# Kernel tuning notes

Hardware: AMD Instinct MI355X
Metric: run time of the kernel (lower is better)

Reference implementation:

```python
import jax, jax.numpy as jnp
import numpy as np

HIDDEN = 300
N_HEADS = 4
DEPTH = 4
N_ATOMS = 30000
N_BONDS = 60000
MAX_NB = 6
N_MOLS = 600
ATOMS_PER_MOL = 50
ATOM_FDIM = 144
BOND_IN = ATOM_FDIM + 14  # 158
W_SCALE = 0.05


def setup_inputs() -> dict:
    key = jax.random.key(0)
    ks = jax.random.split(key, 12)
    rn = lambda k, shp: jax.random.normal(k, shp, dtype=jnp.float32)
    return {
        'fatoms': rn(ks[0], (N_ATOMS, ATOM_FDIM)),
        'fbonds': rn(ks[1], (N_BONDS, BOND_IN)),
        'agraph': jax.random.randint(ks[2], (N_ATOMS, MAX_NB), 0, N_BONDS, dtype=jnp.int32),
        'bgraph': jax.random.randint(ks[3], (N_BONDS, MAX_NB), 0, N_BONDS, dtype=jnp.int32),
        'W_i': rn(ks[4], (HIDDEN, BOND_IN)) * W_SCALE,
        'W_ma': rn(ks[5], (N_HEADS, HIDDEN, HIDDEN)) * W_SCALE,
        'W_h': rn(ks[6], (HIDDEN, N_HEADS * HIDDEN)) * W_SCALE,
        'W_o': rn(ks[7], (HIDDEN, ATOM_FDIM + HIDDEN)) * W_SCALE,
        'b_o': rn(ks[8], (HIDDEN,)) * W_SCALE,
        'W_a': rn(ks[9], (HIDDEN, HIDDEN)) * W_SCALE,
        'W_b': rn(ks[10], (HIDDEN, HIDDEN)) * W_SCALE,
        'b_b': rn(ks[11], (HIDDEN,)) * W_SCALE,
    }


def reference(fatoms, fbonds, agraph, bgraph, W_i, W_ma, W_h, W_o, b_o, W_a, W_b, b_b):
    E, K = bgraph.shape
    NH = W_ma.shape[0]
    H = W_i.shape[0]

    binput = fbonds @ W_i.T                      # [E, H]
    message = jax.nn.relu(binput)
    for _ in range(DEPTH - 1):
        nei = message[bgraph]                    # [E, K, H] gather over neighbor bonds
        # per-head attention scores: <W_ma[n] @ nei_ek, message_e>
        mt = jnp.einsum('eh,nhd->ned', message, W_ma)        # [NH, E, H]
        scores = jnp.einsum('ekd,ned->nek', nei, mt)         # [NH, E, K]
        w = jax.nn.softmax(scores, axis=2)
        comp = jnp.einsum('nek,ekh->enh', w, nei)            # [E, NH, H]
        nei_msg = comp.reshape(E, NH * H) @ W_h.T            # [E, H]
        message = jax.nn.relu(binput + nei_msg)              # dropout(p=0) = identity

    a_nei = message[agraph].sum(axis=1)          # [A, H] gather-sum incoming bonds
    ainput = jnp.concatenate([fatoms, a_nei], axis=1)
    atom_hiddens = jax.nn.relu(ainput @ W_o.T + b_o)         # [A, H]

    # uniform scope: N_MOLS molecules of ATOMS_PER_MOL atoms each
    cur = atom_hiddens.reshape(N_MOLS, ATOMS_PER_MOL, H)
    att_w = jax.nn.softmax(jnp.einsum('mah,mbh->mab', cur @ W_a.T, cur), axis=2)
    att_h = jax.nn.relu(jnp.einsum('mab,mbh->mah', att_w, cur) @ W_b.T + b_b)
    mol_vecs = (cur + att_h).sum(axis=1) / ATOMS_PER_MOL     # [N_MOLS, H]
    return mol_vecs
```

## Files before the change

### kernel.cpp

```cpp
#include <hip/hip_runtime.h>
#include <hip/hip_bf16.h>
#include <math.h>

#define HID       300
#define HP        320
#define NH        4
#define E_BONDS   60000
#define NATOMS    30000
#define KNB       6
#define NMOLS     600
#define APM       50
#define AFD       144
#define BONDIN    158

typedef unsigned short u16;
typedef unsigned int   u32;
typedef _Float16 f16;
typedef f16   f16x8 __attribute__((ext_vector_type(8)));
typedef float f32x4 __attribute__((ext_vector_type(4)));

__device__ inline float hlo(u32 u) { union { u32 i; f16 h[2]; } c; c.i = u; return (float)c.h[0]; }
__device__ inline float hhi(u32 u) { union { u32 i; f16 h[2]; } c; c.i = u; return (float)c.h[1]; }
__device__ inline u32 packh2(float a, float b) {
    union { u32 i; f16 h[2]; } c; c.h[0] = (f16)a; c.h[1] = (f16)b; return c.i;
}

__device__ inline void gl2lds16(const void* g, void* l) {
    __builtin_amdgcn_global_load_lds(
        (const __attribute__((address_space(1))) void*)g,
        (__attribute__((address_space(3))) void*)l, 16, 0, 0);
}

template <int BN, int EPI>
__global__ __launch_bounds__(256) void mfma_gemm_k(
    const f16* __restrict__ A, int lda,
    const f16* __restrict__ B, int ldb,
    int M, int Nb, int K, int ldc,
    float* __restrict__ Cf, f16* __restrict__ Ch,
    const float* __restrict__ bias,
    const f16* __restrict__ resid,
    f16* __restrict__ out2)
{
    constexpr int NF = BN / 32;
    __shared__ f16 sA[128 * 64];
    __shared__ f16 sB[BN * 64];
    const int tid  = threadIdx.x;
    const int lane = tid & 63;
    const int wv   = tid >> 6;
    const int wm   = wv >> 1, wn = wv & 1;
    const int m0   = blockIdx.x * 128, n0 = blockIdx.y * BN;

    f32x4 acc[4][NF];
#pragma unroll
    for (int i = 0; i < 4; ++i)
#pragma unroll
        for (int j = 0; j < NF; ++j) acc[i][j] = (f32x4){0.f, 0.f, 0.f, 0.f};

    for (int k0 = 0; k0 < K; k0 += 64) {
        __syncthreads();
#pragma unroll
        for (int i = 0; i < 4; ++i) {
            int o   = (((i * 4 + wv) * 64) + lane) * 16;
            int row = o >> 7;
            int p   = (o >> 4) & 7;
            int gr  = m0 + row; gr = gr < M ? gr : M - 1;
            const f16* g = A + (size_t)gr * lda + k0 + ((p ^ (row & 7)) << 3);
            gl2lds16(g, (char*)sA + (i * 4 + wv) * 1024);
        }
#pragma unroll
        for (int i = 0; i < BN / 32; ++i) {
            int o   = (((i * 4 + wv) * 64) + lane) * 16;
            int row = o >> 7;
            int p   = (o >> 4) & 7;
            int gr  = n0 + row; gr = gr < Nb ? gr : Nb - 1;
            const f16* g = B + (size_t)gr * ldb + k0 + ((p ^ (row & 7)) << 3);
            gl2lds16(g, (char*)sB + (i * 4 + wv) * 1024);
        }
        __syncthreads();

        const int rl = lane & 15, cl = lane >> 4;
#pragma unroll
        for (int kh = 0; kh < 2; ++kh) {
            f16x8 af[4], bfr[NF];
#pragma unroll
            for (int mf = 0; mf < 4; ++mf) {
                int row = wm * 64 + mf * 16 + rl;
                int ch  = (kh * 4 + cl) ^ (row & 7);
                af[mf]  = *(const f16x8*)&sA[row * 64 + ch * 8];
            }
#pragma unroll
            for (int nf = 0; nf < NF; ++nf) {
                int row = wn * (BN / 2) + nf * 16 + rl;
                int ch  = (kh * 4 + cl) ^ (row & 7);
                bfr[nf] = *(const f16x8*)&sB[row * 64 + ch * 8];
            }
#pragma unroll
            for (int mf = 0; mf < 4; ++mf)
#pragma unroll
                for (int nf = 0; nf < NF; ++nf)
                    acc[mf][nf] = __builtin_amdgcn_mfma_f32_16x16x32_f16(
                        af[mf], bfr[nf], acc[mf][nf], 0, 0, 0);
        }
    }

    const int rl = lane & 15, cl = lane >> 4;
#pragma unroll
    for (int mf = 0; mf < 4; ++mf) {
#pragma unroll
        for (int r = 0; r < 4; ++r) {
            int gm = m0 + wm * 64 + mf * 16 + cl * 4 + r;
            if (gm >= M) continue;
#pragma unroll
            for (int nf = 0; nf < NF; ++nf) {
                int gn = n0 + wn * (BN / 2) + nf * 16 + rl;
                if (gn >= ldc) continue;
                float v = acc[mf][nf][r];
                size_t ci = (size_t)gm * ldc + gn;
                if (EPI == 0) {
                    Cf[ci] = v;
                } else if (EPI == 1) {
                    Ch[ci] = (f16)v;
                } else if (EPI == 2) {
                    Ch[ci] = (f16)v;
                    out2[ci] = (f16)fmaxf(v, 0.f);
                } else if (EPI == 3) {
                    v += (float)resid[ci];
                    Ch[ci] = (f16)fmaxf(v, 0.f);
                } else if (EPI == 4) {
                    v += Cf[ci];
                    v += (gn < HID) ? bias[gn] : 0.f;
                    v = fmaxf(v, 0.f);
                    Cf[ci] = v; Ch[ci] = (f16)v;
                } else {
                    v += (gn < HID) ? bias[gn] : 0.f;
                    Cf[ci] = fmaxf(v, 0.f);
                }
            }
        }
    }
}

__global__ __launch_bounds__(256) void score_comp_k(
    const f16* __restrict__ msg,
    f16* __restrict__ mtc,
    const int* __restrict__ bgraph)
{
    const int tid = threadIdx.x;
    const int e   = blockIdx.x * 16 + (tid >> 4);
    const int t   = tid & 15;

    u32 nei[KNB][10];
#pragma unroll
    for (int k = 0; k < KNB; ++k) {
        int nb = bgraph[e * KNB + k];
        const u32* p = (const u32*)(msg + (size_t)nb * HP) + t * 10;
#pragma unroll
        for (int j = 0; j < 10; ++j) nei[k][j] = p[j];
    }

    for (int n = 0; n < NH; ++n) {
        u32* mrow = (u32*)(mtc + (size_t)e * (NH * HP) + n * HP) + t * 10;
        u32 mt[10];
#pragma unroll
        for (int j = 0; j < 10; ++j) mt[j] = mrow[j];

        float pk[KNB] = {0.f, 0.f, 0.f, 0.f, 0.f, 0.f};
#pragma unroll
        for (int j = 0; j < 10; ++j) {
            float m0 = hlo(mt[j]), m1 = hhi(mt[j]);
#pragma unroll
            for (int k = 0; k < KNB; ++k)
                pk[k] += hlo(nei[k][j]) * m0 + hhi(nei[k][j]) * m1;
        }
#pragma unroll
        for (int s = 1; s < 16; s <<= 1)
#pragma unroll
            for (int k = 0; k < KNB; ++k) pk[k] += __shfl_xor(pk[k], s);

        float mx = pk[0];
#pragma unroll
        for (int k = 1; k < KNB; ++k) mx = fmaxf(mx, pk[k]);
        float w[KNB], sum = 0.f;
#pragma unroll
        for (int k = 0; k < KNB; ++k) { w[k] = __expf(pk[k] - mx); sum += w[k]; }
        float inv = 1.f / sum;
#pragma unroll
        for (int k = 0; k < KNB; ++k) w[k] *= inv;

#pragma unroll
        for (int j = 0; j < 10; ++j) {
            float c0 = 0.f, c1 = 0.f;
#pragma unroll
            for (int k = 0; k < KNB; ++k) {
                c0 += w[k] * hlo(nei[k][j]);
                c1 += w[k] * hhi(nei[k][j]);
            }
            mrow[j] = packh2(c0, c1);
        }
    }
}

__global__ void gather_sum_h_k(const f16* __restrict__ msg,
                               const int* __restrict__ agraph,
                               f16* __restrict__ out) {
    int idx = blockIdx.x * 256 + threadIdx.x;
    if (idx >= NATOMS * (HP / 2)) return;
    int a = idx / (HP / 2), c = idx - a * (HP / 2);
    const int* g = agraph + (size_t)a * KNB;
    float s0 = 0.f, s1 = 0.f;
#pragma unroll
    for (int k = 0; k < KNB; ++k) {
        u32 u = *(const u32*)(msg + (size_t)g[k] * HP + c * 2);
        s0 += hlo(u); s1 += hhi(u);
    }
    ((u32*)out)[idx] = packh2(s0, s1);
}

__global__ void conv_pad_k(const float* __restrict__ src, f16* __restrict__ dst,
                           int R, int C, int CP) {
    int idx = blockIdx.x * 256 + threadIdx.x;
    if (idx >= R * CP) return;
    int r = idx / CP, c = idx - r * CP;
    dst[idx] = (f16)(c < C ? src[(size_t)r * C + c] : 0.f);
}

__global__ void prep_w_k(const float* __restrict__ src, f16* __restrict__ dst,
                         int mode, int R, int CK) {
    int idx = blockIdx.x * 256 + threadIdx.x;
    if (idx >= R * CK) return;
    int r = idx / CK, c = idx - r * CK;
    float v = 0.f;
    if (mode == 0) {
        if (r < HID && c < BONDIN) v = src[r * BONDIN + c];
    } else if (mode == 1) {
        int n = r / HP, d = r - n * HP;
        if (d < HID && c < HID) v = src[((size_t)n * HID + c) * HID + d];
    } else if (mode == 2) {
        int n = c / HP, d = c - n * HP;
        if (r < HID && d < HID) v = src[(size_t)r * (NH * HID) + n * HID + d];
    } else if (mode == 3) {
        if (r < HID && c < AFD) v = src[r * (AFD + HID) + c];
    } else if (mode == 4) {
        if (r < HID && c < HID) v = src[r * (AFD + HID) + AFD + c];
    } else {
        if (r < HID && c < HID) v = src[r * HID + c];
    }
    dst[idx] = (f16)v;
}

__global__ __launch_bounds__(256) void mol_attn_mfma_k(
    const f16* __restrict__ atomHh,
    const f16* __restrict__ ah2h,
    f16* __restrict__ comp2h)
{
    __shared__ f16 sCur[64 * 320];
    __shared__ float sP[64][66];
    const int tid  = threadIdx.x;
    const int lane = tid & 63;
    const int wv   = tid >> 6;
    const int m    = blockIdx.x;
    const int rl   = lane & 15, cl = lane >> 4;

#pragma unroll
    for (int i = 0; i < 10; ++i) {
        int g   = i * 256 + wv * 64 + lane;
        int row = g / 40, c = g - row * 40;
        int grow = m * APM + row; grow = grow < NATOMS ? grow : NATOMS - 1;
        const f16* src = atomHh + (size_t)grow * HP + ((c ^ (row & 7)) << 3);
        gl2lds16(src, (char*)sCur + (size_t)(i * 256 + wv * 64) * 16);
    }
    __syncthreads();

    f32x4 acc[4];
#pragma unroll
    for (int nf = 0; nf < 4; ++nf) acc[nf] = (f32x4){0.f, 0.f, 0.f, 0.f};
    int qrow = m * APM + wv * 16 + rl;
    qrow = qrow < NATOMS ? qrow : NATOMS - 1;
    const f16* qbase = ah2h + (size_t)qrow * HP;
#pragma unroll
    for (int kh = 0; kh < 10; ++kh) {
        f16x8 aq = *(const f16x8*)(qbase + kh * 32 + cl * 8);
#pragma unroll
        for (int nf = 0; nf < 4; ++nf) {
            int brow = nf * 16 + rl;
            int ch   = (kh * 4 + cl) ^ (brow & 7);
            f16x8 bv = *(const f16x8*)&sCur[brow * 320 + ch * 8];
            acc[nf] = __builtin_amdgcn_mfma_f32_16x16x32_f16(aq, bv, acc[nf], 0, 0, 0);
        }
    }

#pragma unroll
    for (int r = 0; r < 4; ++r) {
        float s[4];
#pragma unroll
        for (int nf = 0; nf < 4; ++nf) {
            s[nf] = acc[nf][r];
            if (nf == 3 && rl >= 2) s[nf] = -1e30f;
        }
        float mx = fmaxf(fmaxf(s[0], s[1]), fmaxf(s[2], s[3]));
#pragma unroll
        for (int msk = 1; msk < 16; msk <<= 1) mx = fmaxf(mx, __shfl_xor(mx, msk));
        float e[4], sum = 0.f;
#pragma unroll
        for (int nf = 0; nf < 4; ++nf) { e[nf] = __expf(s[nf] - mx); sum += e[nf]; }
#pragma unroll
        for (int msk = 1; msk < 16; msk <<= 1) sum += __shfl_xor(sum, msk);
        float inv = 1.f / sum;
        int a = wv * 16 + cl * 4 + r;
#pragma unroll
        for (int nf = 0; nf < 4; ++nf) sP[a][nf * 16 + rl] = e[nf] * inv;
    }
    __syncthreads();

    const int a  = tid >> 2, hq = tid & 3;
    const bool aval = a < APM;
    const size_t orow = (size_t)(m * APM + a) * HP;
#pragma unroll
    for (int p = 0; p < 2; ++p) {
        float av[40];
#pragma unroll
        for (int i = 0; i < 40; ++i) av[i] = 0.f;
        const int ch0 = p * 20 + hq * 5;
        for (int b = 0; b < APM; ++b) {
            float w = sP[a][b];
#pragma unroll
            for (int i = 0; i < 5; ++i) {
                int ch = (ch0 + i) ^ (b & 7);
                f16x8 cv = *(const f16x8*)&sCur[b * 320 + ch * 8];
#pragma unroll
                for (int j = 0; j < 8; ++j) av[i * 8 + j] += w * (float)cv[j];
            }
        }
        if (aval) {
#pragma unroll
            for (int i = 0; i < 5; ++i) {
                f16x8 o;
#pragma unroll
                for (int j = 0; j < 8; ++j) o[j] = (f16)av[i * 8 + j];
                *(f16x8*)&comp2h[orow + p * 160 + hq * 40 + i * 8] = o;
            }
        }
    }
}

__global__ void mol_reduce_k(const float* __restrict__ atomH,
                             const float* __restrict__ atth,
                             float* __restrict__ out) {
    const int m = blockIdx.x;
    for (int h = threadIdx.x; h < HID; h += 256) {
        float s = 0.f;
        for (int a = 0; a < APM; ++a) {
            size_t i = (size_t)(m * APM + a) * HP + h;
            s += atomH[i] + atth[i];
        }
        out[(size_t)m * HID + h] = s * (1.f / APM);
    }
}

extern "C" void kernel_launch(void* const* d_in, const int* in_sizes, int n_in,
                              void* d_out, int out_size, void* d_ws, size_t ws_size,
                              hipStream_t stream) {
    const float* fatoms = (const float*)d_in[0];
    const float* fbonds = (const float*)d_in[1];
    const int*   agraph = (const int*)d_in[2];
    const int*   bgraph = (const int*)d_in[3];
    const float* W_i    = (const float*)d_in[4];
    const float* W_ma   = (const float*)d_in[5];
    const float* W_h    = (const float*)d_in[6];
    const float* W_o    = (const float*)d_in[7];
    const float* b_o    = (const float*)d_in[8];
    const float* W_a    = (const float*)d_in[9];
    const float* W_b    = (const float*)d_in[10];
    const float* b_b    = (const float*)d_in[11];
    float* out = (float*)d_out;

    char* ws = (char*)d_ws;
    f16* fbondsh = (f16*)ws;
    f16* mtall   = (f16*)ws;
    f16* aneih   = (f16*)ws;
    f16* fatomsh = (f16*)(ws + 19200000);
    float* atomH = (float*)(ws + 30720000);
    f16* atomHh  = (f16*)(ws + 69120000);
    f16* ah2h    = (f16*)(ws + 88320000);
    f16* comp2h  = (f16*)(ws + 126720000);
    f16* binh    = (f16*)(ws + 153600000);
    float* atth  = (float*)(ws + 153600000);
    f16* msgh    = (f16*)(ws + 192000000);
    char* wb = ws + 230400000;
    f16* WiT  = (f16*)(wb);
    f16* WmaT = (f16*)(wb + 122880);
    f16* WhT  = (f16*)(wb + 942080);
    f16* WoA  = (f16*)(wb + 1761280);
    f16* WoB  = (f16*)(wb + 1884160);
    f16* Wa   = (f16*)(wb + 2088960);
    f16* Wb   = (f16*)(wb + 2293760);

    prep_w_k<<<dim3((320 * 192 + 255) / 256), dim3(256), 0, stream>>>(W_i, WiT, 0, 320, 192);
    prep_w_k<<<dim3((1280 * 320 + 255) / 256), dim3(256), 0, stream>>>(W_ma, WmaT, 1, 1280, 320);
    prep_w_k<<<dim3((320 * 1280 + 255) / 256), dim3(256), 0, stream>>>(W_h, WhT, 2, 320, 1280);
    prep_w_k<<<dim3((320 * 192 + 255) / 256), dim3(256), 0, stream>>>(W_o, WoA, 3, 320, 192);
    prep_w_k<<<dim3((320 * 320 + 255) / 256), dim3(256), 0, stream>>>(W_o, WoB, 4, 320, 320);
    prep_w_k<<<dim3((320 * 320 + 255) / 256), dim3(256), 0, stream>>>(W_a, Wa, 5, 320, 320);
    prep_w_k<<<dim3((320 * 320 + 255) / 256), dim3(256), 0, stream>>>(W_b, Wb, 6, 320, 320);
    conv_pad_k<<<dim3((E_BONDS * 192 + 255) / 256), dim3(256), 0, stream>>>(
        fbonds, fbondsh, E_BONDS, BONDIN, 192);

    mfma_gemm_k<128, 2><<<dim3(469, 3), dim3(256), 0, stream>>>(
        fbondsh, 192, WiT, 192, E_BONDS, 320, 192, HP, nullptr, binh, nullptr, nullptr, msgh);

    for (int it = 0; it < 3; ++it) {
        mfma_gemm_k<128, 1><<<dim3(469, 10), dim3(256), 0, stream>>>(
            msgh, HP, WmaT, HP, E_BONDS, NH * HP, HP, NH * HP, nullptr, mtall, nullptr, nullptr, nullptr);
        score_comp_k<<<dim3(E_BONDS / 16), dim3(256), 0, stream>>>(msgh, mtall, bgraph);
        mfma_gemm_k<128, 3><<<dim3(469, 3), dim3(256), 0, stream>>>(
            mtall, NH * HP, WhT, NH * HP, E_BONDS, HP, NH * HP, HP, nullptr, msgh, nullptr, binh, nullptr);
    }

    gather_sum_h_k<<<dim3((NATOMS * 160 + 255) / 256), dim3(256), 0, stream>>>(msgh, agraph, aneih);
    conv_pad_k<<<dim3((NATOMS * 192 + 255) / 256), dim3(256), 0, stream>>>(
        fatoms, fatomsh, NATOMS, AFD, 192);
    mfma_gemm_k<128, 0><<<dim3(235, 3), dim3(256), 0, stream>>>(
        fatomsh, 192, WoA, 192, NATOMS, 320, 192, HP, atomH, nullptr, nullptr, nullptr, nullptr);
    mfma_gemm_k<128, 4><<<dim3(235, 3), dim3(256), 0, stream>>>(
        aneih, HP, WoB, HP, NATOMS, 320, HP, HP, atomH, atomHh, b_o, nullptr, nullptr);

    mfma_gemm_k<128, 1><<<dim3(235, 3), dim3(256), 0, stream>>>(
        atomHh, HP, Wa, HP, NATOMS, 320, HP, HP, nullptr, ah2h, nullptr, nullptr, nullptr);
    mol_attn_mfma_k<<<dim3(NMOLS), dim3(256), 0, stream>>>(atomHh, ah2h, comp2h);
    mfma_gemm_k<128, 5><<<dim3(235, 3), dim3(256), 0, stream>>>(
        comp2h, HP, Wb, HP, NATOMS, 320, HP, HP, atth, nullptr, b_b, nullptr, nullptr);
    mol_reduce_k<<<dim3(NMOLS), dim3(256), 0, stream>>>(atomH, atth, out);
}
```

Before: 1.122 ms.

## Fuse message-passing GEMMs and attention into one per-iteration kernel

```diff
diff --git a/kernel.cpp b/kernel.cpp
--- a/kernel.cpp
+++ b/kernel.cpp
@@ -140,62 +140,175 @@
     }
 }
 
-__global__ __launch_bounds__(256) void score_comp_k(
-    const f16* __restrict__ msg,
-    f16* __restrict__ mtc,
-    const int* __restrict__ bgraph)
+#define SMC_LD 328
+
+__global__ __launch_bounds__(1024, 1) void fused_mp_k(
+    const f16* __restrict__ msgIn,
+    f16* __restrict__ msgOut,
+    const f16* __restrict__ binh,
+    const int* __restrict__ bgraph,
+    const f16* __restrict__ WmaT,
+    const f16* __restrict__ WhT2)
 {
-    const int tid = threadIdx.x;
-    const int e   = blockIdx.x * 16 + (tid >> 4);
-    const int t   = tid & 15;
-
+    __shared__ f16 sMsg[64 * 320];
+    __shared__ f16 sMC[64 * SMC_LD];
+    __shared__ f16 sB[320 * 64];
+
+    const int tid  = threadIdx.x;
+    const int lane = tid & 63;
+    const int wv   = tid >> 6;
+    const int wm   = wv >> 2;
+    const int wn   = wv & 3;
+    const int rl   = lane & 15, cl = lane >> 4;
+    const int e0   = blockIdx.x * 64;
+
+    const int g = tid >> 4;
+    const int t = tid & 15;
+    int eg = e0 + g; eg = eg < E_BONDS ? eg : E_BONDS - 1;
     u32 nei[KNB][10];
 #pragma unroll
     for (int k = 0; k < KNB; ++k) {
-        int nb = bgraph[e * KNB + k];
-        const u32* p = (const u32*)(msg + (size_t)nb * HP) + t * 10;
+        int nb = bgraph[eg * KNB + k];
+        const u32* p = (const u32*)msgIn + (size_t)nb * (HP / 2) + t * 10;
 #pragma unroll
         for (int j = 0; j < 10; ++j) nei[k][j] = p[j];
     }
 
+#pragma unroll
+    for (int wc = wv; wc < 40; wc += 16) {
+        int q   = wc * 64 + lane;
+        int row = q / 40, c = q - row * 40;
+        int gr  = e0 + row; gr = gr < E_BONDS ? gr : E_BONDS - 1;
+        gl2lds16(msgIn + (size_t)gr * HP + ((c ^ (row & 7)) << 3),
+                 (char*)sMsg + wc * 1024);
+    }
+    __syncthreads();
+
+    f32x4 acc2[5];
+#pragma unroll
+    for (int nf = 0; nf < 5; ++nf) acc2[nf] = (f32x4){0.f, 0.f, 0.f, 0.f};
+
     for (int n = 0; n < NH; ++n) {
-        u32* mrow = (u32*)(mtc + (size_t)e * (NH * HP) + n * HP) + t * 10;
-        u32 mt[10];
-#pragma unroll
-        for (int j = 0; j < 10; ++j) mt[j] = mrow[j];
-
-        float pk[KNB] = {0.f, 0.f, 0.f, 0.f, 0.f, 0.f};
-#pragma unroll
-        for (int j = 0; j < 10; ++j) {
-            float m0 = hlo(mt[j]), m1 = hhi(mt[j]);
-#pragma unroll
-            for (int k = 0; k < KNB; ++k)
-                pk[k] += hlo(nei[k][j]) * m0 + hhi(nei[k][j]) * m1;
-        }
-#pragma unroll
-        for (int s = 1; s < 16; s <<= 1)
-#pragma unroll
-            for (int k = 0; k < KNB; ++k) pk[k] += __shfl_xor(pk[k], s);
-
-        float mx = pk[0];
-#pragma unroll
-        for (int k = 1; k < KNB; ++k) mx = fmaxf(mx, pk[k]);
-        float w[KNB], sum = 0.f;
-#pragma unroll
-        for (int k = 0; k < KNB; ++k) { w[k] = __expf(pk[k] - mx); sum += w[k]; }
-        float inv = 1.f / sum;
-#pragma unroll
-        for (int k = 0; k < KNB; ++k) w[k] *= inv;
-
-#pragma unroll
-        for (int j = 0; j < 10; ++j) {
-            float c0 = 0.f, c1 = 0.f;
-#pragma unroll
-            for (int k = 0; k < KNB; ++k) {
-                c0 += w[k] * hlo(nei[k][j]);
-                c1 += w[k] * hhi(nei[k][j]);
-            }
-            mrow[j] = packh2(c0, c1);
+        const f16* B1 = WmaT + (size_t)n * HP * HP;
+        f32x4 acc1[5];
+#pragma unroll
+        for (int nf = 0; nf < 5; ++nf) acc1[nf] = (f32x4){0.f, 0.f, 0.f, 0.f};
+
+        for (int kc = 0; kc < 5; ++kc) {
+            __syncthreads();
+#pragma unroll
+            for (int wc = wv; wc < 40; wc += 16) {
+                int q = wc * 64 + lane;
+                int brow = q >> 3, c = q & 7;
+                gl2lds16(B1 + (size_t)brow * HP + kc * 64 + ((c ^ (brow & 7)) << 3),
+                         (char*)sB + wc * 1024);
+            }
+            __syncthreads();
+#pragma unroll
+            for (int lk = 0; lk < 2; ++lk) {
+                int arow = wm * 16 + rl;
+                int ach  = (kc * 8 + lk * 4 + cl) ^ (rl & 7);
+                f16x8 a  = *(const f16x8*)&sMsg[arow * HP + ach * 8];
+#pragma unroll
+                for (int nf = 0; nf < 5; ++nf) {
+                    int brow = (wn + nf * 4) * 16 + rl;
+                    int bch  = (lk * 4 + cl) ^ (rl & 7);
+                    f16x8 b  = *(const f16x8*)&sB[brow * 64 + bch * 8];
+                    acc1[nf] = __builtin_amdgcn_mfma_f32_16x16x32_f16(a, b, acc1[nf], 0, 0, 0);
+                }
+            }
+        }
+#pragma unroll
+        for (int nf = 0; nf < 5; ++nf) {
+#pragma unroll
+            for (int r = 0; r < 4; ++r) {
+                int row = wm * 16 + cl * 4 + r;
+                int col = (wn + nf * 4) * 16 + rl;
+                sMC[row * SMC_LD + col] = (f16)acc1[nf][r];
+            }
+        }
+        __syncthreads();
+
+        {
+            const u32* mp = (const u32*)&sMC[g * SMC_LD + t * 20];
+            u32 mtv[10];
+#pragma unroll
+            for (int j = 0; j < 10; ++j) mtv[j] = mp[j];
+
+            float pk[KNB] = {0.f, 0.f, 0.f, 0.f, 0.f, 0.f};
+#pragma unroll
+            for (int j = 0; j < 10; ++j) {
+                float m0 = hlo(mtv[j]), m1 = hhi(mtv[j]);
+#pragma unroll
+                for (int k = 0; k < KNB; ++k)
+                    pk[k] += hlo(nei[k][j]) * m0 + hhi(nei[k][j]) * m1;
+            }
+#pragma unroll
+            for (int s = 1; s < 16; s <<= 1)
+#pragma unroll
+                for (int k = 0; k < KNB; ++k) pk[k] += __shfl_xor(pk[k], s);
+
+            float mx = pk[0];
+#pragma unroll
+            for (int k = 1; k < KNB; ++k) mx = fmaxf(mx, pk[k]);
+            float w[KNB], sum = 0.f;
+#pragma unroll
+            for (int k = 0; k < KNB; ++k) { w[k] = __expf(pk[k] - mx); sum += w[k]; }
+            float inv = 1.f / sum;
+#pragma unroll
+            for (int k = 0; k < KNB; ++k) w[k] *= inv;
+
+            u32* cp = (u32*)&sMC[g * SMC_LD + t * 20];
+#pragma unroll
+            for (int j = 0; j < 10; ++j) {
+                float c0 = 0.f, c1 = 0.f;
+#pragma unroll
+                for (int k = 0; k < KNB; ++k) {
+                    c0 += w[k] * hlo(nei[k][j]);
+                    c1 += w[k] * hhi(nei[k][j]);
+                }
+                cp[j] = packh2(c0, c1);
+            }
+        }
+        __syncthreads();
+
+        const f16* B2 = WhT2 + (size_t)n * HP * HP;
+        for (int kc = 0; kc < 5; ++kc) {
+            __syncthreads();
+#pragma unroll
+            for (int wc = wv; wc < 40; wc += 16) {
+                int q = wc * 64 + lane;
+                int brow = q >> 3, c = q & 7;
+                gl2lds16(B2 + (size_t)brow * HP + kc * 64 + ((c ^ (brow & 7)) << 3),
+                         (char*)sB + wc * 1024);
+            }
+            __syncthreads();
+#pragma unroll
+            for (int lk = 0; lk < 2; ++lk) {
+                int arow = wm * 16 + rl;
+                f16x8 a  = *(const f16x8*)&sMC[arow * SMC_LD + kc * 64 + lk * 32 + cl * 8];
+#pragma unroll
+                for (int nf = 0; nf < 5; ++nf) {
+                    int brow = (wn + nf * 4) * 16 + rl;
+                    int bch  = (lk * 4 + cl) ^ (rl & 7);
+                    f16x8 b  = *(const f16x8*)&sB[brow * 64 + bch * 8];
+                    acc2[nf] = __builtin_amdgcn_mfma_f32_16x16x32_f16(a, b, acc2[nf], 0, 0, 0);
+                }
+            }
+        }
+        __syncthreads();
+    }
+
+#pragma unroll
+    for (int nf = 0; nf < 5; ++nf) {
+#pragma unroll
+        for (int r = 0; r < 4; ++r) {
+            int gm = e0 + wm * 16 + cl * 4 + r;
+            if (gm >= E_BONDS) continue;
+            int col = (wn + nf * 4) * 16 + rl;
+            size_t ci = (size_t)gm * HP + col;
+            float v = acc2[nf][r] + (float)binh[ci];
+            msgOut[ci] = (f16)fmaxf(v, 0.f);
         }
     }
 }
@@ -236,8 +349,8 @@
         int n = r / HP, d = r - n * HP;
         if (d < HID && c < HID) v = src[((size_t)n * HID + c) * HID + d];
     } else if (mode == 2) {
-        int n = c / HP, d = c - n * HP;
-        if (r < HID && d < HID) v = src[(size_t)r * (NH * HID) + n * HID + d];
+        int n = r / HP, h = r - n * HP;
+        if (h < HID && c < HID) v = src[(size_t)h * (NH * HID) + n * HID + c];
     } else if (mode == 3) {
         if (r < HID && c < AFD) v = src[r * (AFD + HID) + c];
     } else if (mode == 4) {
@@ -375,21 +488,21 @@
     float* out = (float*)d_out;
 
     char* ws = (char*)d_ws;
-    f16* fbondsh = (f16*)ws;
-    f16* mtall   = (f16*)ws;
-    f16* aneih   = (f16*)ws;
-    f16* fatomsh = (f16*)(ws + 19200000);
-    float* atomH = (float*)(ws + 30720000);
-    f16* atomHh  = (f16*)(ws + 69120000);
-    f16* ah2h    = (f16*)(ws + 88320000);
-    f16* comp2h  = (f16*)(ws + 126720000);
-    f16* binh    = (f16*)(ws + 153600000);
-    float* atth  = (float*)(ws + 153600000);
-    f16* msgh    = (f16*)(ws + 192000000);
-    char* wb = ws + 230400000;
+    f16* msgA    = (f16*)(ws);
+    f16* msgB    = (f16*)(ws + 38400000);
+    f16* binh    = (f16*)(ws + 76800000);
+    f16* fbondsh = (f16*)(ws + 115200000);
+    f16* aneih   = (f16*)(ws);
+    f16* fatomsh = (f16*)(ws + 38400000);
+    float* atomH = (float*)(ws + 76800000);
+    f16* atomHh  = (f16*)(ws + 115200000);
+    f16* ah2h    = (f16*)(ws + 134400000);
+    f16* comp2h  = (f16*)(ws + 153600000);
+    float* atth  = (float*)(ws + 172800000);
+    char* wb = ws + 211200000;
     f16* WiT  = (f16*)(wb);
     f16* WmaT = (f16*)(wb + 122880);
-    f16* WhT  = (f16*)(wb + 942080);
+    f16* WhT2 = (f16*)(wb + 942080);
     f16* WoA  = (f16*)(wb + 1761280);
     f16* WoB  = (f16*)(wb + 1884160);
     f16* Wa   = (f16*)(wb + 2088960);
@@ -397,7 +510,7 @@
 
     prep_w_k<<<dim3((320 * 192 + 255) / 256), dim3(256), 0, stream>>>(W_i, WiT, 0, 320, 192);
     prep_w_k<<<dim3((1280 * 320 + 255) / 256), dim3(256), 0, stream>>>(W_ma, WmaT, 1, 1280, 320);
-    prep_w_k<<<dim3((320 * 1280 + 255) / 256), dim3(256), 0, stream>>>(W_h, WhT, 2, 320, 1280);
+    prep_w_k<<<dim3((1280 * 320 + 255) / 256), dim3(256), 0, stream>>>(W_h, WhT2, 2, 1280, 320);
     prep_w_k<<<dim3((320 * 192 + 255) / 256), dim3(256), 0, stream>>>(W_o, WoA, 3, 320, 192);
     prep_w_k<<<dim3((320 * 320 + 255) / 256), dim3(256), 0, stream>>>(W_o, WoB, 4, 320, 320);
     prep_w_k<<<dim3((320 * 320 + 255) / 256), dim3(256), 0, stream>>>(W_a, Wa, 5, 320, 320);
@@ -406,17 +519,13 @@
         fbonds, fbondsh, E_BONDS, BONDIN, 192);
 
     mfma_gemm_k<128, 2><<<dim3(469, 3), dim3(256), 0, stream>>>(
-        fbondsh, 192, WiT, 192, E_BONDS, 320, 192, HP, nullptr, binh, nullptr, nullptr, msgh);
-
-    for (int it = 0; it < 3; ++it) {
-        mfma_gemm_k<128, 1><<<dim3(469, 10), dim3(256), 0, stream>>>(
-            msgh, HP, WmaT, HP, E_BONDS, NH * HP, HP, NH * HP, nullptr, mtall, nullptr, nullptr, nullptr);
-        score_comp_k<<<dim3(E_BONDS / 16), dim3(256), 0, stream>>>(msgh, mtall, bgraph);
-        mfma_gemm_k<128, 3><<<dim3(469, 3), dim3(256), 0, stream>>>(
-            mtall, NH * HP, WhT, NH * HP, E_BONDS, HP, NH * HP, HP, nullptr, msgh, nullptr, binh, nullptr);
-    }
-
-    gather_sum_h_k<<<dim3((NATOMS * 160 + 255) / 256), dim3(256), 0, stream>>>(msgh, agraph, aneih);
+        fbondsh, 192, WiT, 192, E_BONDS, 320, 192, HP, nullptr, binh, nullptr, nullptr, msgA);
+
+    fused_mp_k<<<dim3(938), dim3(1024), 0, stream>>>(msgA, msgB, binh, bgraph, WmaT, WhT2);
+    fused_mp_k<<<dim3(938), dim3(1024), 0, stream>>>(msgB, msgA, binh, bgraph, WmaT, WhT2);
+    fused_mp_k<<<dim3(938), dim3(1024), 0, stream>>>(msgA, msgB, binh, bgraph, WmaT, WhT2);
+
+    gather_sum_h_k<<<dim3((NATOMS * 160 + 255) / 256), dim3(256), 0, stream>>>(msgB, agraph, aneih);
     conv_pad_k<<<dim3((NATOMS * 192 + 255) / 256), dim3(256), 0, stream>>>(
         fatoms, fatomsh, NATOMS, AFD, 192);
     mfma_gemm_k<128, 0><<<dim3(235, 3), dim3(256), 0, stream>>>(
```

After: 3.093 ms. 176% more time.
